# Optimization experiments

Measured on AMD Instinct MI355X. Metric: run time of the kernel, lower is better.

## Reference

```python
import jax, jax.numpy as jnp
import numpy as np

B, T, N, M, D = 4, 64, 16, 8, 512

def setup_inputs() -> dict:
    key = jax.random.key(0)
    ks = jax.random.split(key, 7)
    s = 1.0 / np.sqrt(D)
    return {
        "x": jax.random.normal(ks[0], (B, T, N, M, D), dtype=jnp.float32),
        "Wq": jax.random.normal(ks[1], (D, D), dtype=jnp.float32) * s,
        "bq": jax.random.normal(ks[2], (D,), dtype=jnp.float32) * s,
        "Wk": jax.random.normal(ks[3], (D, D), dtype=jnp.float32) * s,
        "bk": jax.random.normal(ks[4], (D,), dtype=jnp.float32) * s,
        "Wv": jax.random.normal(ks[5], (D, D), dtype=jnp.float32) * s,
        "bv": jax.random.normal(ks[6], (D,), dtype=jnp.float32) * s,
    }

def reference(x, Wq, bq, Wk, bk, Wv, bv):
    # Linear projections (torch Linear: y = x @ W^T + b)
    Q = jnp.einsum('btnmd,ed->btnme', x, Wq) + bq
    K = jnp.einsum('btnmd,ed->btnme', x, Wk) + bk
    V = jnp.einsum('btnmd,ed->btnme', x, Wv) + bv
    scale = 1.0 / jnp.sqrt(jnp.asarray(Q.shape[-1], Q.dtype))
    # contract over batch b AND feature d -> shared attention over modality axis m
    attn_score = jnp.einsum('btnmd,btnkd->tnmk', Q, K) * scale  # [t,n,m,m]
    attn_weight = jax.nn.softmax(attn_score, axis=-1)
    return jnp.einsum('tnmk,btnkd->btnmd', attn_weight, V)
```

## Files before the change

### kernel.cpp

```cpp
#include <hip/hip_runtime.h>

#define Bb 4
#define Tt 64
#define Nn 16
#define Mm 8
#define Dd 512
#define RR 32
#define QSTR 536
#define VOFF 270336

typedef __attribute__((ext_vector_type(8))) short bf16x8;
typedef __attribute__((ext_vector_type(16))) float f32x16;

__device__ __forceinline__ unsigned short f2bf(float f) {
    union { float f; unsigned int u; } v; v.f = f;
    unsigned int r = (v.u + 0x7fffu + ((v.u >> 16) & 1u)) >> 16;
    return (unsigned short)r;
}
__device__ __forceinline__ float bf2f(unsigned short h) {
    union { unsigned int u; float f; } v; v.u = ((unsigned int)h) << 16;
    return v.f;
}

__global__ __launch_bounds__(256) void pack_kernel(
    const float* __restrict__ Wq, const float* __restrict__ Wk,
    const float* __restrict__ Wv, const float* __restrict__ bq,
    unsigned short* __restrict__ Wb)
{
    const int tid = threadIdx.x;
    if (blockIdx.x >= 256) {
        int idx = (blockIdx.x - 256) * 256 + tid;
        int o = idx << 2;
        int j  = o & 7;
        int n  = (o >> 3) & 31;
        int hi = (o >> 8) & 1;
        int ekk = o >> 9;
        int kk = ekk & 31;
        int e  = ekk >> 5;
        int row = e * 32 + n;
        int d = kk * 16 + hi * 8 + j;
        float4 v = *(const float4*)(Wv + row * Dd + d);
        ushort4 o4;
        o4.x = f2bf(v.x); o4.y = f2bf(v.y); o4.z = f2bf(v.z); o4.w = f2bf(v.w);
        *(ushort4*)(Wb + VOFF + o) = o4;
        return;
    }

    const int eT = blockIdx.x & 15;
    const int dT = blockIdx.x >> 4;
    const int wave = tid >> 6, lane = tid & 63;
    const int arow = lane & 31, h = lane >> 5;

    f32x16 acc;
    #pragma unroll
    for (int r = 0; r < 16; ++r) acc[r] = 0.f;

    #pragma unroll
    for (int s = 0; s < 8; ++s) {
        int n0 = (wave * 8 + s) * 16;
        bf16x8 af, bfr;
        #pragma unroll
        for (int j = 0; j < 8; ++j) {
            int n = n0 + h * 8 + j;
            af[j]  = (short)f2bf(Wq[n * Dd + dT * 32 + arow]);
            bfr[j] = (short)f2bf(Wk[n * Dd + eT * 32 + arow]);
        }
        acc = __builtin_amdgcn_mfma_f32_32x32x16_bf16(af, bfr, acc, 0, 0, 0);
    }

    __shared__ float red[4][1024];
    #pragma unroll
    for (int r = 0; r < 16; ++r) {
        int row = (r & 3) + 8 * (r >> 2) + 4 * h;
        red[wave][row * 32 + arow] = acc[r];
    }
    __syncthreads();

    #pragma unroll
    for (int i = 0; i < 4; ++i) {
        int el = i * 256 + tid;
        int dp = el >> 5, ep = el & 31;
        float v = red[0][el] + red[1][el] + red[2][el] + red[3][el];
        int d = dT * 32 + dp;
        int kkg = d >> 4, hh = (d >> 3) & 1, jj = d & 7;
        Wb[(long)(eT * 33 + kkg) * 512 + ((hh * 32 + ep) << 3) + jj] = f2bf(v);
    }

    if (dT == 0) {
        int ep = tid & 31, strip = tid >> 5;
        float c = 0.f;
        #pragma unroll 8
        for (int n = strip * 64; n < strip * 64 + 64; ++n)
            c += bf2f(f2bf(Wk[n * Dd + eT * 32 + ep])) * bq[n];
        __syncthreads();
        red[0][tid] = c;
        long b32 = (long)(eT * 33 + 32) << 9;
        Wb[b32 + tid] = 0; Wb[b32 + 256 + tid] = 0;
        __syncthreads();
        if (tid < 32) {
            float s = 0.f;
            #pragma unroll
            for (int k = 0; k < 8; ++k) s += red[0][k * 32 + tid];
            Wb[b32 + (tid << 3)] = f2bf(s);
        }
    }
}

__global__ __launch_bounds__(1024, 4) void fused_attn_kernel(
    const float* __restrict__ x, const unsigned short* __restrict__ Wb,
    const float* __restrict__ bv, float* __restrict__ out)
{
    __shared__ unsigned short lds_x[2][RR * QSTR];
    __shared__ float lds_s[2][64];

    const int tid = threadIdx.x;
    const int lane = tid & 63;
    const int wave = tid >> 6;
    const int arow = lane & 31;
    const int ahalf = lane >> 5;
    const int l5 = lane & 31;

    const int gi0 = blockIdx.x << 1;
    const int t = gi0 >> 4;
    const int n0 = gi0 & 15;
    const int rot = (blockIdx.x * 7) & 31;

    const unsigned short* wb = Wb + (long)wave * (33 * 512) + (lane << 3);
    #define KOF(s) ((s) + rot >= 32 ? (s) + rot - 32 : (s) + rot)

    bf16x8 pf[6];
    #pragma unroll
    for (int i = 0; i < 6; ++i)
        pf[i] = *(const bf16x8*)(wb + KOF(i) * 512);

    if (tid < 128) lds_s[tid >> 6][tid & 63] = 0.f;

    #pragma unroll
    for (int i = 0; i < 8; ++i) {
        int fi = i * 1024 + tid;
        int g = fi >> 12;
        int rem = fi & 4095;
        int row = rem >> 7;
        int d = (rem & 127) << 2;
        int b = row >> 3, m = row & 7;
        float4 v = *(const float4*)(x + ((((long)(b * Tt + t)) * Nn + (n0 + g)) * Mm + m) * Dd + d);
        ushort4 o;
        o.x = f2bf(v.x); o.y = f2bf(v.y); o.z = f2bf(v.z); o.w = f2bf(v.w);
        *(ushort4*)(&lds_x[g][row * QSTR + d]) = o;
    }
    if (tid < 64) {
        int g = tid >> 5, row = tid & 31;
        unsigned short* p = &lds_x[g][row * QSTR + 512];
        ushort4 one = {0x3F80, 0, 0, 0}, zz = {0, 0, 0, 0};
        *(ushort4*)(p) = one; *(ushort4*)(p + 4) = zz;
        *(ushort4*)(p + 8) = zz; *(ushort4*)(p + 12) = zz;
    }
    __syncthreads();

    const unsigned short* abase0 = &lds_x[0][arow * QSTR + (ahalf << 3)];
    const unsigned short* abase1 = &lds_x[1][arow * QSTR + (ahalf << 3)];

    f32x16 aY0, aY1;
    #pragma unroll
    for (int r = 0; r < 16; ++r) { aY0[r] = 0.f; aY1[r] = 0.f; }

    #pragma unroll
    for (int s = 0; s < 33; ++s) {
        int kk = (s < 32) ? KOF(s) : 32;
        bf16x8 bf = pf[s % 6];
        if (s + 6 <= 32) {
            int kn = (s + 6 < 32) ? KOF(s + 6) : 32;
            pf[s % 6] = *(const bf16x8*)(wb + kn * 512);
        }
        bf16x8 a0 = *(const bf16x8*)(abase0 + kk * 16);
        bf16x8 a1 = *(const bf16x8*)(abase1 + kk * 16);
        aY0 = __builtin_amdgcn_mfma_f32_32x32x16_bf16(a0, bf, aY0, 0, 0, 0);
        aY1 = __builtin_amdgcn_mfma_f32_32x32x16_bf16(a1, bf, aY1, 0, 0, 0);
    }

    const int ecol = (wave << 5) + l5;
    #pragma unroll
    for (int g = 0; g < 2; ++g) {
        const f32x16& aY = g ? aY1 : aY0;
        float p[32];
        #pragma unroll
        for (int i = 0; i < 32; ++i) p[i] = 0.f;
        #pragma unroll
        for (int b = 0; b < 4; ++b) {
            float xc[8];
            #pragma unroll
            for (int k = 0; k < 8; ++k)
                xc[k] = bf2f(lds_x[g][(b * 8 + k) * QSTR + ecol]);
            #pragma unroll
            for (int mm = 0; mm < 4; ++mm) {
                float yv = aY[b * 4 + mm];
                #pragma unroll
                for (int k = 0; k < 8; ++k) p[mm * 8 + k] += yv * xc[k];
            }
        }
        const bool b0 = (lane & 1) != 0;
        const bool b1 = (lane & 2) != 0;
        const bool b2 = (lane & 4) != 0;
        const bool b3 = (lane & 8) != 0;
        const bool b4 = (lane & 16) != 0;
        float q16[16];
        #pragma unroll
        for (int i = 0; i < 16; ++i) {
            float keep = b0 ? p[2 * i + 1] : p[2 * i];
            float send = b0 ? p[2 * i] : p[2 * i + 1];
            q16[i] = keep + __shfl_xor(send, 1);
        }
        float q8[8];
        #pragma unroll
        for (int i = 0; i < 8; ++i) {
            float keep = b1 ? q16[2 * i + 1] : q16[2 * i];
            float send = b1 ? q16[2 * i] : q16[2 * i + 1];
            q8[i] = keep + __shfl_xor(send, 2);
        }
        float q4[4];
        #pragma unroll
        for (int i = 0; i < 4; ++i) {
            float keep = b2 ? q8[2 * i + 1] : q8[2 * i];
            float send = b2 ? q8[2 * i] : q8[2 * i + 1];
            q4[i] = keep + __shfl_xor(send, 4);
        }
        float q2[2];
        #pragma unroll
        for (int i = 0; i < 2; ++i) {
            float keep = b3 ? q4[2 * i + 1] : q4[2 * i];
            float send = b3 ? q4[2 * i] : q4[2 * i + 1];
            q2[i] = keep + __shfl_xor(send, 8);
        }
        float sval = (b4 ? q2[1] : q2[0]) + __shfl_xor(b4 ? q2[0] : q2[1], 16);
        int k = l5 & 7, mm = l5 >> 3;
        int m = mm + 4 * ahalf;
        atomicAdd(&lds_s[g][m * 8 + k], sval);
    }

    const unsigned short* vb = Wb + VOFF + ((long)wave << 14) + (lane << 3);
    bf16x8 pv[4];
    pv[0] = *(const bf16x8*)(vb + ((0 + rot) & 31) * 512);
    pv[1] = *(const bf16x8*)(vb + ((1 + rot) & 31) * 512);
    pv[2] = *(const bf16x8*)(vb + ((2 + rot) & 31) * 512);
    pv[3] = *(const bf16x8*)(vb + ((3 + rot) & 31) * 512);

    __syncthreads();

    if (tid < 128) {
        int g = tid >> 6;
        int p = tid & 63;
        float s = lds_s[g][p] * 0.04419417382415922f;
        float mx = s;
        mx = fmaxf(mx, __shfl_xor(mx, 1));
        mx = fmaxf(mx, __shfl_xor(mx, 2));
        mx = fmaxf(mx, __shfl_xor(mx, 4));
        float e = __expf(s - mx);
        float sum = e;
        sum += __shfl_xor(sum, 1);
        sum += __shfl_xor(sum, 2);
        sum += __shfl_xor(sum, 4);
        lds_s[g][p] = e / sum;
    }
    __syncthreads();

    {
        int d4 = tid & 127;
        int b = (tid >> 7) & 3;
        int g = tid >> 9;
        unsigned short* xr = &lds_x[g][(b << 3) * QSTR + (d4 << 2)];
        float4 xv[8];
        #pragma unroll
        for (int k = 0; k < 8; ++k) {
            ushort4 u = *(const ushort4*)(xr + k * QSTR);
            xv[k].x = bf2f(u.x); xv[k].y = bf2f(u.y);
            xv[k].z = bf2f(u.z); xv[k].w = bf2f(u.w);
        }
        ushort4 yr[8];
        #pragma unroll
        for (int m = 0; m < 8; ++m) {
            float4 o = {0.f, 0.f, 0.f, 0.f};
            #pragma unroll
            for (int k = 0; k < 8; ++k) {
                float w = lds_s[g][(m << 3) + k];
                o.x += w * xv[k].x; o.y += w * xv[k].y;
                o.z += w * xv[k].z; o.w += w * xv[k].w;
            }
            ushort4 oy;
            oy.x = f2bf(o.x); oy.y = f2bf(o.y); oy.z = f2bf(o.z); oy.w = f2bf(o.w);
            yr[m] = oy;
        }
        #pragma unroll
        for (int m = 0; m < 8; ++m) *(ushort4*)(xr + m * QSTR) = yr[m];
    }
    __syncthreads();

    {
        f32x16 aV0, aV1;
        #pragma unroll
        for (int r = 0; r < 16; ++r) { aV0[r] = 0.f; aV1[r] = 0.f; }
        #pragma unroll
        for (int s = 0; s < 32; ++s) {
            int kk = (s + rot) & 31;
            bf16x8 wvf = pv[s & 3];
            if (s + 4 < 32) pv[s & 3] = *(const bf16x8*)(vb + (((s + 4 + rot) & 31)) * 512);
            bf16x8 a0 = *(const bf16x8*)(abase0 + kk * 16);
            bf16x8 a1 = *(const bf16x8*)(abase1 + kk * 16);
            aV0 = __builtin_amdgcn_mfma_f32_32x32x16_bf16(a0, wvf, aV0, 0, 0, 0);
            aV1 = __builtin_amdgcn_mfma_f32_32x32x16_bf16(a1, wvf, aV1, 0, 0, 0);
        }
        int f = (wave << 5) + arow;
        float bvv = bv[f];
        float* o0 = out + f;
        #pragma unroll
        for (int r = 0; r < 16; ++r) {
            int mrow = (r & 3) + 8 * (r >> 2) + 4 * ahalf;
            int b = mrow >> 3, m = mrow & 7;
            long base = ((((long)(b * Tt + t)) * Nn + n0) * Mm + m) * Dd;
            o0[base] = aV0[r] + bvv;
            o0[base + (long)Mm * Dd] = aV1[r] + bvv;
        }
    }
    #undef KOF
}

extern "C" void kernel_launch(void* const* d_in, const int* in_sizes, int n_in,
                              void* d_out, int out_size, void* d_ws, size_t ws_size,
                              hipStream_t stream) {
    const float* x  = (const float*)d_in[0];
    const float* Wq = (const float*)d_in[1];
    const float* bq = (const float*)d_in[2];
    const float* Wk = (const float*)d_in[3];
    const float* Wv = (const float*)d_in[5];
    const float* bv = (const float*)d_in[6];
    float* out = (float*)d_out;
    unsigned short* Wb = (unsigned short*)d_ws;

    pack_kernel<<<512, 256, 0, stream>>>(Wq, Wk, Wv, bq, Wb);
    fused_attn_kernel<<<Tt * Nn / 2, 1024, 0, stream>>>(x, Wb, bv, out);
}
```

Before: 169.4 us.

## Compute V projection before softmax and mix attention weights in registers

The V projection (x·Wv) now runs right after the score GEMM, before the softmax barrier. The attention-weighted mixing is then applied to the V accumulators in registers, using a cross-half lane shuffle, instead of first mixing x in LDS and then running the V GEMM. This removes the LDS mix pass and one barrier and lets the V MFMAs overlap the wait on the score reduction. It also shrinks the Q/K weight prefetch depth from 6 to 4 and raises the launch-bounds occupancy hint from 4 to 8, which could force register spills given the larger live state. Rounding also changes: the mix now happens in fp32 on the projected values instead of in bf16 on x.

```diff
diff --git a/kernel.cpp b/kernel.cpp
--- a/kernel.cpp
+++ b/kernel.cpp
@@ -106,7 +106,7 @@
     }
 }
 
-__global__ __launch_bounds__(1024, 4) void fused_attn_kernel(
+__global__ __launch_bounds__(1024, 8) void fused_attn_kernel(
     const float* __restrict__ x, const unsigned short* __restrict__ Wb,
     const float* __restrict__ bv, float* __restrict__ out)
 {
@@ -128,9 +128,9 @@
     const unsigned short* wb = Wb + (long)wave * (33 * 512) + (lane << 3);
     #define KOF(s) ((s) + rot >= 32 ? (s) + rot - 32 : (s) + rot)
 
-    bf16x8 pf[6];
-    #pragma unroll
-    for (int i = 0; i < 6; ++i)
+    bf16x8 pf[4];
+    #pragma unroll
+    for (int i = 0; i < 4; ++i)
         pf[i] = *(const bf16x8*)(wb + KOF(i) * 512);
 
     if (tid < 128) lds_s[tid >> 6][tid & 63] = 0.f;
@@ -167,16 +167,23 @@
     #pragma unroll
     for (int s = 0; s < 33; ++s) {
         int kk = (s < 32) ? KOF(s) : 32;
-        bf16x8 bf = pf[s % 6];
-        if (s + 6 <= 32) {
-            int kn = (s + 6 < 32) ? KOF(s + 6) : 32;
-            pf[s % 6] = *(const bf16x8*)(wb + kn * 512);
+        bf16x8 bf = pf[s & 3];
+        if (s + 4 <= 32) {
+            int kn = (s + 4 < 32) ? KOF(s + 4) : 32;
+            pf[s & 3] = *(const bf16x8*)(wb + kn * 512);
         }
         bf16x8 a0 = *(const bf16x8*)(abase0 + kk * 16);
         bf16x8 a1 = *(const bf16x8*)(abase1 + kk * 16);
         aY0 = __builtin_amdgcn_mfma_f32_32x32x16_bf16(a0, bf, aY0, 0, 0, 0);
         aY1 = __builtin_amdgcn_mfma_f32_32x32x16_bf16(a1, bf, aY1, 0, 0, 0);
     }
+
+    const unsigned short* vb = Wb + VOFF + ((long)wave << 14) + (lane << 3);
+    bf16x8 pv[4];
+    pv[0] = *(const bf16x8*)(vb + ((0 + rot) & 31) * 512);
+    pv[1] = *(const bf16x8*)(vb + ((1 + rot) & 31) * 512);
+    pv[2] = *(const bf16x8*)(vb + ((2 + rot) & 31) * 512);
+    pv[3] = *(const bf16x8*)(vb + ((3 + rot) & 31) * 512);
 
     const int ecol = (wave << 5) + l5;
     #pragma unroll
@@ -237,13 +244,19 @@
         atomicAdd(&lds_s[g][m * 8 + k], sval);
     }
 
-    const unsigned short* vb = Wb + VOFF + ((long)wave << 14) + (lane << 3);
-    bf16x8 pv[4];
-    pv[0] = *(const bf16x8*)(vb + ((0 + rot) & 31) * 512);
-    pv[1] = *(const bf16x8*)(vb + ((1 + rot) & 31) * 512);
-    pv[2] = *(const bf16x8*)(vb + ((2 + rot) & 31) * 512);
-    pv[3] = *(const bf16x8*)(vb + ((3 + rot) & 31) * 512);
-
+    f32x16 aZ0, aZ1;
+    #pragma unroll
+    for (int r = 0; r < 16; ++r) { aZ0[r] = 0.f; aZ1[r] = 0.f; }
+    #pragma unroll
+    for (int s = 0; s < 32; ++s) {
+        int kk = (s + rot) & 31;
+        bf16x8 wvf = pv[s & 3];
+        if (s + 4 < 32) pv[s & 3] = *(const bf16x8*)(vb + (((s + 4 + rot) & 31)) * 512);
+        bf16x8 a0 = *(const bf16x8*)(abase0 + kk * 16);
+        bf16x8 a1 = *(const bf16x8*)(abase1 + kk * 16);
+        aZ0 = __builtin_amdgcn_mfma_f32_32x32x16_bf16(a0, wvf, aZ0, 0, 0, 0);
+        aZ1 = __builtin_amdgcn_mfma_f32_32x32x16_bf16(a1, wvf, aZ1, 0, 0, 0);
+    }
     __syncthreads();
 
     if (tid < 128) {
@@ -264,60 +277,31 @@
     __syncthreads();
 
     {
-        int d4 = tid & 127;
-        int b = (tid >> 7) & 3;
-        int g = tid >> 9;
-        unsigned short* xr = &lds_x[g][(b << 3) * QSTR + (d4 << 2)];
-        float4 xv[8];
-        #pragma unroll
-        for (int k = 0; k < 8; ++k) {
-            ushort4 u = *(const ushort4*)(xr + k * QSTR);
-            xv[k].x = bf2f(u.x); xv[k].y = bf2f(u.y);
-            xv[k].z = bf2f(u.z); xv[k].w = bf2f(u.w);
-        }
-        ushort4 yr[8];
-        #pragma unroll
-        for (int m = 0; m < 8; ++m) {
-            float4 o = {0.f, 0.f, 0.f, 0.f};
-            #pragma unroll
-            for (int k = 0; k < 8; ++k) {
-                float w = lds_s[g][(m << 3) + k];
-                o.x += w * xv[k].x; o.y += w * xv[k].y;
-                o.z += w * xv[k].z; o.w += w * xv[k].w;
-            }
-            ushort4 oy;
-            oy.x = f2bf(o.x); oy.y = f2bf(o.y); oy.z = f2bf(o.z); oy.w = f2bf(o.w);
-            yr[m] = oy;
-        }
-        #pragma unroll
-        for (int m = 0; m < 8; ++m) *(ushort4*)(xr + m * QSTR) = yr[m];
-    }
-    __syncthreads();
-
-    {
-        f32x16 aV0, aV1;
-        #pragma unroll
-        for (int r = 0; r < 16; ++r) { aV0[r] = 0.f; aV1[r] = 0.f; }
-        #pragma unroll
-        for (int s = 0; s < 32; ++s) {
-            int kk = (s + rot) & 31;
-            bf16x8 wvf = pv[s & 3];
-            if (s + 4 < 32) pv[s & 3] = *(const bf16x8*)(vb + (((s + 4 + rot) & 31)) * 512);
-            bf16x8 a0 = *(const bf16x8*)(abase0 + kk * 16);
-            bf16x8 a1 = *(const bf16x8*)(abase1 + kk * 16);
-            aV0 = __builtin_amdgcn_mfma_f32_32x32x16_bf16(a0, wvf, aV0, 0, 0, 0);
-            aV1 = __builtin_amdgcn_mfma_f32_32x32x16_bf16(a1, wvf, aV1, 0, 0, 0);
-        }
         int f = (wave << 5) + arow;
         float bvv = bv[f];
         float* o0 = out + f;
         #pragma unroll
-        for (int r = 0; r < 16; ++r) {
-            int mrow = (r & 3) + 8 * (r >> 2) + 4 * ahalf;
-            int b = mrow >> 3, m = mrow & 7;
-            long base = ((((long)(b * Tt + t)) * Nn + n0) * Mm + m) * Dd;
-            o0[base] = aV0[r] + bvv;
-            o0[base + (long)Mm * Dd] = aV1[r] + bvv;
+        for (int g = 0; g < 2; ++g) {
+            const f32x16& z = g ? aZ1 : aZ0;
+            float zs[16];
+            #pragma unroll
+            for (int r = 0; r < 16; ++r) zs[r] = __shfl_xor(z[r], 32);
+            #pragma unroll
+            for (int j = 0; j < 4; ++j) {
+                int m = j + 4 * ahalf;
+                float4 pA = *(const float4*)&lds_s[g][m * 8 + 4 * ahalf];
+                float4 pB = *(const float4*)&lds_s[g][m * 8 + 4 * (1 - ahalf)];
+                #pragma unroll
+                for (int b = 0; b < 4; ++b) {
+                    int r0 = 4 * b;
+                    float o = pA.x * z[r0]  + pA.y * z[r0 + 1]
+                            + pA.z * z[r0 + 2] + pA.w * z[r0 + 3]
+                            + pB.x * zs[r0] + pB.y * zs[r0 + 1]
+                            + pB.z * zs[r0 + 2] + pB.w * zs[r0 + 3];
+                    long base = ((((long)(b * Tt + t)) * Nn + (n0 + g)) * Mm + m) * Dd;
+                    o0[base] = o + bvv;
+                }
+            }
         }
     }
     #undef KOF
```

Result: slower. 200.3 us (+18.2%).
